# Optimization experiments

Hardware: AMD Instinct MI355X
Metric: run time of the kernel (lower is better)

The kernel has to match this reference:

```python
import jax, jax.numpy as jnp
import numpy as np
from jax import lax

NSTEPS = 7
BN_EPS = 1e-5


def setup_inputs() -> dict:
    key = jax.random.key(0)
    ks = jax.random.split(key, 7)
    bs, in_ch, h, w, k = 8, 16, 256, 256, 3
    f = jax.random.normal(ks[0], (bs, in_ch, h, w), dtype=jnp.float32)
    vec_w = jax.random.normal(ks[1], (2 * in_ch, in_ch, k, k), dtype=jnp.float32) * 0.1
    vec_b = jax.random.normal(ks[2], (2 * in_ch,), dtype=jnp.float32) * 0.1
    bn_gamma = jnp.ones((2 * in_ch,), dtype=jnp.float32)
    bn_beta = jnp.zeros((2 * in_ch,), dtype=jnp.float32)
    fuse_w = jax.random.normal(ks[3], (in_ch, in_ch, NSTEPS, 1, 1), dtype=jnp.float32) * 0.1
    fuse_b = jax.random.normal(ks[4], (in_ch,), dtype=jnp.float32) * 0.1
    return {"f": f, "vec_w": vec_w, "vec_b": vec_b, "bn_gamma": bn_gamma,
            "bn_beta": bn_beta, "fuse_w": fuse_w, "fuse_b": fuse_b}


def _bilinear_sample(src, py, px):
    """Bilinear sample with zero padding (torch grid_sample align_corners=True).
    src: [N,C,H,W]; py,px: [N,H,W] pixel coordinates (row, col)."""
    N, C, H, W = src.shape
    y0 = jnp.floor(py); x0 = jnp.floor(px)
    wy1 = py - y0; wy0 = 1.0 - wy1
    wx1 = px - x0; wx0 = 1.0 - wx1
    src_flat = src.reshape(N, C, H * W)

    def gather(yi, xi):
        valid = (yi >= 0) & (yi <= H - 1) & (xi >= 0) & (xi <= W - 1)
        yc = jnp.clip(yi, 0, H - 1).astype(jnp.int32)
        xc = jnp.clip(xi, 0, W - 1).astype(jnp.int32)
        idx = (yc * W + xc).reshape(N, 1, H * W)
        vals = jnp.take_along_axis(src_flat, idx, axis=2).reshape(N, C, H, W)
        return vals * valid.astype(src.dtype)[:, None, :, :]

    out = (wy0 * wx0)[:, None] * gather(y0, x0) \
        + (wy0 * wx1)[:, None] * gather(y0, x0 + 1) \
        + (wy1 * wx0)[:, None] * gather(y0 + 1, x0) \
        + (wy1 * wx1)[:, None] * gather(y0 + 1, x0 + 1)
    return out


def _warp(src, flow, grid_y, grid_x):
    # grid + flow in pixel space; original normalizes to [-1,1] then grid_sample
    # un-normalizes with align_corners=True, which is exactly pixel coords grid+flow.
    py = grid_y[None] + flow[:, 0]
    px = grid_x[None] + flow[:, 1]
    return _bilinear_sample(src, py, px)


def reference(f, vec_w, vec_b, bn_gamma, bn_beta, fuse_w, fuse_b):
    bs, in_ch, h, w = f.shape
    # vec_conv + BatchNorm2d (training-mode batch stats, biased variance)
    vec = lax.conv_general_dilated(f, vec_w, (1, 1), [(1, 1), (1, 1)],
                                   dimension_numbers=("NCHW", "OIHW", "NCHW"))
    vec = vec + vec_b[None, :, None, None]
    mean = vec.mean(axis=(0, 2, 3))
    var = vec.var(axis=(0, 2, 3))
    vec = bn_gamma[None, :, None, None] * (vec - mean[None, :, None, None]) \
        * lax.rsqrt(var + BN_EPS)[None, :, None, None] + bn_beta[None, :, None, None]

    c = vec.shape[1]  # = 2*in_ch
    vec = vec.reshape(bs * c // 2, 2, h, w)  # per-channel 2D flow fields

    grid_y, grid_x = jnp.meshgrid(jnp.arange(h, dtype=f.dtype),
                                  jnp.arange(w, dtype=f.dtype), indexing="ij")

    # VecInt: scaling and squaring, keeping every intermediate deformation
    vec = vec * (1.0 / 2 ** NSTEPS)
    deforms = []
    for _ in range(NSTEPS):
        vec = vec + _warp(vec, vec, grid_y, grid_x)
        deforms.append(vec)

    fsrc = f.reshape(bs * in_ch, 1, h, w)
    maps = [_warp(fsrc, d, grid_y, grid_x).reshape(bs, in_ch, h, w) for d in deforms]
    stacked = jnp.stack(maps, axis=2)  # [bs, in_ch, nsteps, h, w]

    # Conv3d with kernel (nsteps,1,1) then squeeze -> per-pixel channel/step mix
    out = jnp.einsum("ocs,bcshw->bohw", fuse_w[:, :, :, 0, 0], stacked)
    out = out + fuse_b[None, :, None, None]
    return out
```

## Files before the change

kernel.cpp:

```cpp
#include <hip/hip_runtime.h>
#include <hip/hip_fp16.h>

#define H 256
#define W 256
#define BS 8
#define IC 16
#define OCH 32
#define NSTEPS 7
#define PLANE (H*W)
#define NFIELDS (BS*IC)
#define BN_N (BS*PLANE)
#define BN_EPS 1e-5f
#define PW 260
#define PSZ (260 * 260)

__global__ void transpose_w_kernel(const float* __restrict__ w,
                                   __half2* __restrict__ wTh) {
    for (int idx = threadIdx.x; idx < IC * 9 * 16; idx += blockDim.x) {
        int rc = idx >> 4;
        int p  = idx & 15;
        float lo = w[(2 * p) * (IC * 9) + rc];
        float hi = w[(2 * p + 1) * (IC * 9) + rc];
        wTh[idx] = __floats2half2_rn(lo, hi);
    }
}

__global__ void guard_zero_kernel(unsigned* __restrict__ bufA,
                                  unsigned* __restrict__ bufB,
                                  unsigned short* __restrict__ f16p) {
    int p = blockIdx.x;
    size_t pb = (size_t)p * PSZ;
    for (int i = threadIdx.x; i < 2064; i += blockDim.x) {
        int row, col;
        if (i < 1040) {
            int r = i / 260;
            row = (r == 0) ? 0 : 256 + r;
            col = i - r * 260;
        } else {
            int j = i - 1040;
            int c = j / 256;
            col = (c == 0) ? 0 : 256 + c;
            row = 1 + (j - c * 256);
        }
        size_t off = pb + (size_t)row * PW + col;
        bufA[off] = 0u;
        bufB[off] = 0u;
        f16p[off] = 0;
    }
}

__global__ __launch_bounds__(256) void dup_kernel(const float* __restrict__ f,
                                                  __half* __restrict__ f16p) {
    int blk = blockIdx.x;
    int p  = blk >> 3;
    int r0 = (blk & 7) * 32;
    const float* fp = f + (size_t)p * PLANE;
    __half* dp = f16p + (size_t)p * PSZ;
    int tx = threadIdx.x;
#pragma unroll 4
    for (int ry = 0; ry < 32; ++ry) {
        int y = r0 + ry;
        dp[(size_t)(y + 1) * PW + tx + 1] = __float2half(fp[(size_t)y * W + tx]);
    }
}

__global__ __launch_bounds__(256, 8) void conv_kernel(
    const float* __restrict__ f, const __half2* __restrict__ wTh,
    const float* __restrict__ vec_b, __half2* __restrict__ vec_out) {
    __shared__ __align__(16) __half sf[16][10][40];

    int blk = blockIdx.x;
    int xcd = blk & 7;
    int i   = blk >> 3;
    int b   = i >> 5;
    int j   = i & 31;
    int ty0 = ((xcd << 2) | (j >> 3)) * 8;
    int tx0 = (j & 7) * 32;
    int tid = threadIdx.x;

    {
        int sic = tid >> 4;
        int st  = tid & 15;
        if (st < 10) {
            int gx0 = tx0 - 4 + 4 * st;
            const float* fpl = f + (size_t)(b * IC + sic) * PLANE;
            bool full = (gx0 >= 0) && (gx0 + 3 < W);
#pragma unroll
            for (int r = 0; r < 10; ++r) {
                int gy = ty0 - 1 + r;
                float4 v = make_float4(0.f, 0.f, 0.f, 0.f);
                if ((unsigned)gy < (unsigned)H) {
                    if (full) {
                        v = *(const float4*)(fpl + (size_t)gy * W + gx0);
                    } else {
                        if ((unsigned)(gx0 + 0) < (unsigned)W) v.x = fpl[(size_t)gy * W + gx0 + 0];
                        if ((unsigned)(gx0 + 1) < (unsigned)W) v.y = fpl[(size_t)gy * W + gx0 + 1];
                        if ((unsigned)(gx0 + 2) < (unsigned)W) v.z = fpl[(size_t)gy * W + gx0 + 2];
                        if ((unsigned)(gx0 + 3) < (unsigned)W) v.w = fpl[(size_t)gy * W + gx0 + 3];
                    }
                }
                union { __half2 h[2]; float2 f2; } u;
                u.h[0] = __floats2half2_rn(v.x, v.y);
                u.h[1] = __floats2half2_rn(v.z, v.w);
                *(float2*)&sf[sic][r][4 * st] = u.f2;
            }
        }
    }

    __half2 acc[16];
#pragma unroll
    for (int p = 0; p < 16; ++p)
        acc[p] = __floats2half2_rn(vec_b[2 * p], vec_b[2 * p + 1]);

    __syncthreads();

    int tyl = tid >> 5, txl = tid & 31;
#pragma unroll 2
    for (int ic = 0; ic < 16; ++ic) {
#pragma unroll
        for (int k = 0; k < 9; ++k) {
            int ky = k / 3, kx = k - ky * 3;
            __half2 fv = __half2half2(sf[ic][tyl + ky][txl + kx + 3]);
            const __half2* wrow = wTh + (ic * 9 + k) * 16;
#pragma unroll
            for (int p = 0; p < 16; ++p)
                acc[p] = __hfma2(fv, wrow[p], acc[p]);
        }
    }

    int y = ty0 + tyl, x = tx0 + txl;
#pragma unroll
    for (int c = 0; c < IC; ++c)
        vec_out[(size_t)(b * IC + c) * PLANE + (size_t)y * W + x] = acc[c];
}

__global__ __launch_bounds__(256) void stats_kernel(
    const __half2* __restrict__ vec, float* __restrict__ stats) {
    int blk   = blockIdx.x;
    int n     = blk >> 4;
    int chunk = blk & 15;
    const float4* p4 = (const float4*)(vec + (size_t)n * PLANE + chunk * 4096);
    int tid = threadIdx.x;

    float s0 = 0.f, s1 = 0.f, q0 = 0.f, q1 = 0.f;
#pragma unroll 2
    for (int i = tid; i < 1024; i += 256) {
        float4 w = p4[i];
        const __half2* hh = (const __half2*)&w;
#pragma unroll
        for (int q = 0; q < 4; ++q) {
            float2 v = __half22float2(hh[q]);
            s0 += v.x; s1 += v.y;
            q0 = fmaf(v.x, v.x, q0);
            q1 = fmaf(v.y, v.y, q1);
        }
    }
#pragma unroll
    for (int off = 32; off > 0; off >>= 1) {
        s0 += __shfl_down(s0, off, 64);
        s1 += __shfl_down(s1, off, 64);
        q0 += __shfl_down(q0, off, 64);
        q1 += __shfl_down(q1, off, 64);
    }
    __shared__ float red[4][4];
    int wave = tid >> 6, lane = tid & 63;
    if (lane == 0) {
        red[wave][0] = s0; red[wave][1] = s1;
        red[wave][2] = q0; red[wave][3] = q1;
    }
    __syncthreads();
    if (tid == 0) {
        float t0 = 0.f, t1 = 0.f, t2 = 0.f, t3 = 0.f;
#pragma unroll
        for (int wv = 0; wv < 4; ++wv) {
            t0 += red[wv][0]; t1 += red[wv][1];
            t2 += red[wv][2]; t3 += red[wv][3];
        }
        int ch0 = 2 * (n & 15);
        atomicAdd(stats + ch0,          t0);
        atomicAdd(stats + ch0 + 1,      t1);
        atomicAdd(stats + 32 + ch0,     t2);
        atomicAdd(stats + 32 + ch0 + 1, t3);
    }
}

__global__ void finalize_kernel(const float* __restrict__ stats,
                                const float* __restrict__ gamma,
                                const float* __restrict__ beta,
                                float* __restrict__ AB) {
    int ch = threadIdx.x;
    if (ch < 2 * IC) {
        const float invN = 1.f / (float)BN_N;
        float mean = stats[ch] * invN;
        float var  = stats[32 + ch] * invN - mean * mean;
        float rs   = rsqrtf(var + BN_EPS);
        float a    = gamma[ch] * rs;
        AB[ch]      = a * (1.f / 128.f);
        AB[32 + ch] = (beta[ch] - a * mean) * (1.f / 128.f);
    }
}

__device__ __forceinline__ void tap_setup(float py, float px,
                                          int* o, float* wt) {
    float ffy = floorf(py), ffx = floorf(px);
    int y0 = (int)ffy, x0 = (int)ffx;
    float wy1 = py - ffy, wy0 = 1.f - wy1;
    float wx1 = px - ffx, wx0 = 1.f - wx1;
    bool vy0 = (unsigned)y0 < (unsigned)H, vy1 = (unsigned)(y0 + 1) < (unsigned)H;
    bool vx0 = (unsigned)x0 < (unsigned)W, vx1 = (unsigned)(x0 + 1) < (unsigned)W;
    int yc0 = min(max(y0, 0), H - 1), yc1 = min(max(y0 + 1, 0), H - 1);
    int xc0 = min(max(x0, 0), W - 1), xc1 = min(max(x0 + 1, 0), W - 1);
    o[0] = yc0 * W + xc0; o[1] = yc0 * W + xc1;
    o[2] = yc1 * W + xc0; o[3] = yc1 * W + xc1;
    wt[0] = (vy0 && vx0) ? wy0 * wx0 : 0.f;
    wt[1] = (vy0 && vx1) ? wy0 * wx1 : 0.f;
    wt[2] = (vy1 && vx0) ? wy1 * wx0 : 0.f;
    wt[3] = (vy1 && vx1) ? wy1 * wx1 : 0.f;
}

__device__ __forceinline__ void tap_fast(float py, float px,
                                         int& o, float* wt) {
    float pyc = fminf(fmaxf(py, -1.f), 256.f);
    float pxc = fminf(fmaxf(px, -1.f), 256.f);
    float fy = floorf(pyc), fx = floorf(pxc);
    int y0 = (int)fy, x0 = (int)fx;
    float wy1 = pyc - fy, wy0 = 1.f - wy1;
    float wx1 = pxc - fx, wx0 = 1.f - wx1;
    o = (y0 + 1) * PW + (x0 + 1);
    wt[0] = wy0 * wx0; wt[1] = wy0 * wx1;
    wt[2] = wy1 * wx0; wt[3] = wy1 * wx1;
}

template <bool FIRST, bool LAST>
__global__ __launch_bounds__(256) void step_kernel(
    const __half2* __restrict__ vinRaw, const __half2* __restrict__ vinPad,
    __half2* __restrict__ voutPad, const __half* __restrict__ f16p,
    const float* __restrict__ AB, const float* __restrict__ fw,
    const float* __restrict__ fb, __half* __restrict__ accp,
    float* __restrict__ out, int step) {
    int blk = blockIdx.x;
    int xcd = blk & 7;
    int i   = blk >> 3;
    int b   = i >> 5;
    int h   = (xcd << 5) | (i & 31);
    int tx  = threadIdx.x;
    int idx_raw = h * W + tx;
    int idx_pad = (h + 1) * PW + tx + 1;
    const size_t baseR = (size_t)b * IC * PLANE;
    const size_t baseP = (size_t)b * IC * PSZ;

    float mv[IC];

#pragma unroll 2
    for (int g = 0; g < 4; ++g) {
        float a0j[4], b0j[4], a1j[4], b1j[4];
        float fy[4], fx[4];
        float wt[4][4];
        int   ob[4];
        int   om[4][4];
        const __half2* pl[4];
        float2 vc[4];

#pragma unroll
        for (int j = 0; j < 4; ++j) {
            int c = 4 * g + j;
            if (FIRST) {
                pl[j] = vinRaw + baseR + (size_t)c * PLANE;
                vc[j] = __half22float2(pl[j][idx_raw]);
            } else {
                pl[j] = vinPad + baseP + (size_t)c * PSZ;
                vc[j] = __half22float2(pl[j][idx_pad]);
            }
        }

#pragma unroll
        for (int j = 0; j < 4; ++j) {
            int c = 4 * g + j;
            if (FIRST) {
                a0j[j] = AB[2 * c];     b0j[j] = AB[32 + 2 * c];
                a1j[j] = AB[2 * c + 1]; b1j[j] = AB[32 + 2 * c + 1];
                fy[j] = fmaf(a0j[j], vc[j].x, b0j[j]);
                fx[j] = fmaf(a1j[j], vc[j].y, b1j[j]);
                tap_setup((float)h + fy[j], (float)tx + fx[j], om[j], wt[j]);
            } else {
                fy[j] = vc[j].x;
                fx[j] = vc[j].y;
                tap_fast((float)h + fy[j], (float)tx + fx[j], ob[j], wt[j]);
            }
        }

        float2 t[4][4];
#pragma unroll
        for (int j = 0; j < 4; ++j) {
            if (FIRST) {
#pragma unroll
                for (int k = 0; k < 4; ++k)
                    t[j][k] = __half22float2(pl[j][om[j][k]]);
            } else {
                union { float2 f2; __half2 hh[2]; } top, bot;
                top.f2 = *reinterpret_cast<const float2*>(pl[j] + ob[j]);
                bot.f2 = *reinterpret_cast<const float2*>(pl[j] + ob[j] + PW);
                t[j][0] = __half22float2(top.hh[0]);
                t[j][1] = __half22float2(top.hh[1]);
                t[j][2] = __half22float2(bot.hh[0]);
                t[j][3] = __half22float2(bot.hh[1]);
            }
        }

        float ny[4], nx[4];
        int   pb_[4];
        float pw_[4][4];
#pragma unroll
        for (int j = 0; j < 4; ++j) {
            int c = 4 * g + j;
            float Sy = wt[j][0] * t[j][0].x + wt[j][1] * t[j][1].x
                     + wt[j][2] * t[j][2].x + wt[j][3] * t[j][3].x;
            float Sx = wt[j][0] * t[j][0].y + wt[j][1] * t[j][1].y
                     + wt[j][2] * t[j][2].y + wt[j][3] * t[j][3].y;
            if (FIRST) {
                float Ws = wt[j][0] + wt[j][1] + wt[j][2] + wt[j][3];
                ny[j] = fy[j] + fmaf(a0j[j], Sy, b0j[j] * Ws);
                nx[j] = fx[j] + fmaf(a1j[j], Sx, b1j[j] * Ws);
            } else {
                ny[j] = fy[j] + Sy;
                nx[j] = fx[j] + Sx;
            }
            if (!LAST)
                voutPad[baseP + (size_t)c * PSZ + idx_pad] =
                    __float22half2_rn(make_float2(ny[j], nx[j]));
            tap_fast((float)h + ny[j], (float)tx + nx[j], pb_[j], pw_[j]);
        }

#pragma unroll
        for (int j = 0; j < 4; ++j) {
            int c = 4 * g + j;
            const __half* fp = f16p + baseP + (size_t)c * PSZ;
            union { float f; __half2 h; } r0, r1;
            r0.f = *reinterpret_cast<const float*>(fp + pb_[j]);
            r1.f = *reinterpret_cast<const float*>(fp + pb_[j] + PW);
            float2 g0 = __half22float2(r0.h);
            float2 g1 = __half22float2(r1.h);
            mv[c] = pw_[j][0] * g0.x + pw_[j][1] * g0.y
                  + pw_[j][2] * g1.x + pw_[j][3] * g1.y;
        }
    }

    __half* ap = accp + ((size_t)b * PLANE + idx_raw) * IC;
    float prev[IC];
    if (!FIRST) {
        float4 p0 = ((const float4*)ap)[0];
        float4 p1 = ((const float4*)ap)[1];
        const __half2* ph = (const __half2*)&p0;
#pragma unroll
        for (int k = 0; k < 4; ++k) {
            float2 v = __half22float2(ph[k]);
            prev[2 * k] = v.x; prev[2 * k + 1] = v.y;
        }
        const __half2* qh = (const __half2*)&p1;
#pragma unroll
        for (int k = 0; k < 4; ++k) {
            float2 v = __half22float2(qh[k]);
            prev[8 + 2 * k] = v.x; prev[8 + 2 * k + 1] = v.y;
        }
    }

    float a[IC];
#pragma unroll
    for (int o2 = 0; o2 < IC; ++o2) {
        a[o2] = FIRST ? fb[o2] : prev[o2];
#pragma unroll
        for (int c = 0; c < IC; ++c)
            a[o2] = fmaf(fw[(o2 * IC + c) * NSTEPS + step], mv[c], a[o2]);
    }

    if (LAST) {
#pragma unroll
        for (int o2 = 0; o2 < IC; ++o2)
            out[baseR + (size_t)o2 * PLANE + idx_raw] = a[o2];
    } else {
        float4 s0, s1;
        __half2* sh = (__half2*)&s0;
#pragma unroll
        for (int k = 0; k < 4; ++k)
            sh[k] = __float22half2_rn(make_float2(a[2 * k], a[2 * k + 1]));
        __half2* th = (__half2*)&s1;
#pragma unroll
        for (int k = 0; k < 4; ++k)
            th[k] = __float22half2_rn(make_float2(a[8 + 2 * k], a[9 + 2 * k]));
        ((float4*)ap)[0] = s0;
        ((float4*)ap)[1] = s1;
    }
}

extern "C" void kernel_launch(void* const* d_in, const int* in_sizes, int n_in,
                              void* d_out, int out_size, void* d_ws,
                              size_t ws_size, hipStream_t stream) {
    const float* f      = (const float*)d_in[0];
    const float* vec_w  = (const float*)d_in[1];
    const float* vec_b  = (const float*)d_in[2];
    const float* gamma  = (const float*)d_in[3];
    const float* beta   = (const float*)d_in[4];
    const float* fuse_w = (const float*)d_in[5];
    const float* fuse_b = (const float*)d_in[6];
    float* out = (float*)d_out;

    char* ws = (char*)d_ws;
    const size_t rawB  = (size_t)NFIELDS * PLANE * sizeof(__half2);
    const size_t padB2 = (size_t)NFIELDS * PSZ * sizeof(__half2);
    const size_t padB1 = (size_t)NFIELDS * PSZ * sizeof(__half);
    const size_t accB  = (size_t)NFIELDS * PLANE * sizeof(__half);
    __half2* bufRaw = (__half2*)ws;
    __half2* bufA   = (__half2*)(ws + rawB);
    __half2* bufB   = (__half2*)(ws + rawB + padB2);
    __half*  f16p   = (__half*)(ws + rawB + 2 * padB2);
    __half*  accp   = (__half*)(ws + rawB + 2 * padB2 + padB1);
    __half2* wTh    = (__half2*)(ws + rawB + 2 * padB2 + padB1 + accB);
    float*   stats  = (float*)(wTh + IC * 9 * 16);
    float*   AB     = stats + 64;

    hipMemsetAsync(stats, 0, 64 * sizeof(float), stream);
    transpose_w_kernel<<<1, 512, 0, stream>>>(vec_w, wTh);
    guard_zero_kernel<<<NFIELDS, 256, 0, stream>>>(
        (unsigned*)bufA, (unsigned*)bufB, (unsigned short*)f16p);
    dup_kernel<<<NFIELDS * 8, 256, 0, stream>>>(f, f16p);
    conv_kernel<<<2048, 256, 0, stream>>>(f, wTh, vec_b, bufRaw);
    stats_kernel<<<NFIELDS * 16, 256, 0, stream>>>(bufRaw, stats);
    finalize_kernel<<<1, 64, 0, stream>>>(stats, gamma, beta, AB);

    for (int s = 0; s < NSTEPS; ++s) {
        const __half2* vinPad = (s & 1) ? bufA : bufB;
        __half2*       voutP  = (s & 1) ? bufB : bufA;
        if (s == 0)
            step_kernel<true, false><<<2048, 256, 0, stream>>>(
                bufRaw, (const __half2*)nullptr, bufA, f16p, AB,
                fuse_w, fuse_b, accp, out, s);
        else if (s < NSTEPS - 1)
            step_kernel<false, false><<<2048, 256, 0, stream>>>(
                (const __half2*)nullptr, vinPad, voutP, f16p, AB,
                fuse_w, fuse_b, accp, out, s);
        else
            step_kernel<false, true><<<2048, 256, 0, stream>>>(
                (const __half2*)nullptr, vinPad, (__half2*)nullptr, f16p, AB,
                fuse_w, fuse_b, accp, out, s);
    }
}
```

Before: 502.4 us.

## Split warp steps from channel mix, storing per-step warped maps for a final mix kernel

```diff
diff --git a/kernel.cpp b/kernel.cpp
--- a/kernel.cpp
+++ b/kernel.cpp
@@ -232,6 +232,111 @@
 }
 
 template <bool FIRST, bool LAST>
+__global__ __launch_bounds__(256, 4) void warp_step(
+    const __half2* __restrict__ vinRaw, const __half2* __restrict__ vinPad,
+    __half2* __restrict__ voutPad, const __half* __restrict__ f16p,
+    const float* __restrict__ AB, __half* __restrict__ mvOut) {
+    int blk  = blockIdx.x;
+    int fld  = blk & 127;
+    int band = blk >> 7;
+    int c    = fld & 15;
+    int tx   = threadIdx.x;
+    const __half2* vinR = FIRST ? vinRaw + (size_t)fld * PLANE : nullptr;
+    const __half2* vinP = FIRST ? nullptr : vinPad + (size_t)fld * PSZ;
+    __half2* voutP = LAST ? nullptr : voutPad + (size_t)fld * PSZ;
+    const __half* fp = f16p + (size_t)fld * PSZ;
+    __half* mv = mvOut + (size_t)fld * PLANE;
+
+    float a0 = 0.f, b0 = 0.f, a1 = 0.f, b1 = 0.f;
+    if (FIRST) {
+        a0 = AB[2 * c];     b0 = AB[32 + 2 * c];
+        a1 = AB[2 * c + 1]; b1 = AB[32 + 2 * c + 1];
+    }
+
+#pragma unroll 4
+    for (int r = 0; r < 8; ++r) {
+        int h = band * 8 + r;
+        int idx_raw = h * W + tx;
+        int idx_pad = (h + 1) * PW + tx + 1;
+        float ny, nx;
+        if (FIRST) {
+            float2 vc = __half22float2(vinR[idx_raw]);
+            float fy = fmaf(a0, vc.x, b0);
+            float fx = fmaf(a1, vc.y, b1);
+            int om[4]; float wt[4];
+            tap_setup((float)h + fy, (float)tx + fx, om, wt);
+            float2 t0 = __half22float2(vinR[om[0]]);
+            float2 t1 = __half22float2(vinR[om[1]]);
+            float2 t2 = __half22float2(vinR[om[2]]);
+            float2 t3 = __half22float2(vinR[om[3]]);
+            float Sy = wt[0] * t0.x + wt[1] * t1.x + wt[2] * t2.x + wt[3] * t3.x;
+            float Sx = wt[0] * t0.y + wt[1] * t1.y + wt[2] * t2.y + wt[3] * t3.y;
+            float Ws = wt[0] + wt[1] + wt[2] + wt[3];
+            ny = fy + fmaf(a0, Sy, b0 * Ws);
+            nx = fx + fmaf(a1, Sx, b1 * Ws);
+        } else {
+            float2 vc = __half22float2(vinP[idx_pad]);
+            float fy = vc.x, fx = vc.y;
+            int ob; float wt[4];
+            tap_fast((float)h + fy, (float)tx + fx, ob, wt);
+            union { float2 f2; __half2 hh[2]; } top, bot;
+            top.f2 = *reinterpret_cast<const float2*>(vinP + ob);
+            bot.f2 = *reinterpret_cast<const float2*>(vinP + ob + PW);
+            float2 t0 = __half22float2(top.hh[0]);
+            float2 t1 = __half22float2(top.hh[1]);
+            float2 t2 = __half22float2(bot.hh[0]);
+            float2 t3 = __half22float2(bot.hh[1]);
+            ny = fy + wt[0] * t0.x + wt[1] * t1.x + wt[2] * t2.x + wt[3] * t3.x;
+            nx = fx + wt[0] * t0.y + wt[1] * t1.y + wt[2] * t2.y + wt[3] * t3.y;
+        }
+        if (!LAST)
+            voutP[idx_pad] = __float22half2_rn(make_float2(ny, nx));
+        int pb; float pw[4];
+        tap_fast((float)h + ny, (float)tx + nx, pb, pw);
+        union { float f; __half2 h2; } r0u, r1u;
+        r0u.f = *reinterpret_cast<const float*>(fp + pb);
+        r1u.f = *reinterpret_cast<const float*>(fp + pb + PW);
+        float2 g0 = __half22float2(r0u.h2);
+        float2 g1 = __half22float2(r1u.h2);
+        float m = pw[0] * g0.x + pw[1] * g0.y + pw[2] * g1.x + pw[3] * g1.y;
+        mv[idx_raw] = __float2half(m);
+    }
+}
+
+__global__ __launch_bounds__(256) void mix_kernel(
+    const __half* __restrict__ mvs,
+    const __half* __restrict__ mv6,
+    const float* __restrict__ fw, const float* __restrict__ fb,
+    float* __restrict__ out) {
+    int blk = blockIdx.x;
+    int b   = blk >> 8;
+    int h   = blk & 255;
+    int tx  = threadIdx.x;
+    int idx = h * W + tx;
+
+    float acc[IC];
+#pragma unroll
+    for (int o = 0; o < IC; ++o) acc[o] = fb[o];
+
+#pragma unroll
+    for (int s = 0; s < NSTEPS; ++s) {
+        const __half* base = (s < NSTEPS - 1)
+            ? mvs + (size_t)s * NFIELDS * PLANE : mv6;
+#pragma unroll
+        for (int c = 0; c < IC; ++c) {
+            float m = __half2float(base[(size_t)(b * IC + c) * PLANE + idx]);
+#pragma unroll
+            for (int o = 0; o < IC; ++o)
+                acc[o] = fmaf(fw[(o * IC + c) * NSTEPS + s], m, acc[o]);
+        }
+    }
+
+#pragma unroll
+    for (int o = 0; o < IC; ++o)
+        out[(size_t)(b * IC + o) * PLANE + idx] = acc[o];
+}
+
+template <bool FIRST, bool LAST>
 __global__ __launch_bounds__(256) void step_kernel(
     const __half2* __restrict__ vinRaw, const __half2* __restrict__ vinPad,
     __half2* __restrict__ voutPad, const __half* __restrict__ f16p,
@@ -405,18 +510,26 @@
     float* out = (float*)d_out;
 
     char* ws = (char*)d_ws;
-    const size_t rawB  = (size_t)NFIELDS * PLANE * sizeof(__half2);
-    const size_t padB2 = (size_t)NFIELDS * PSZ * sizeof(__half2);
-    const size_t padB1 = (size_t)NFIELDS * PSZ * sizeof(__half);
-    const size_t accB  = (size_t)NFIELDS * PLANE * sizeof(__half);
+    const size_t rawB   = (size_t)NFIELDS * PLANE * sizeof(__half2);
+    const size_t padB2  = (size_t)NFIELDS * PSZ * sizeof(__half2);
+    const size_t padB1  = (size_t)NFIELDS * PSZ * sizeof(__half);
+    const size_t planeH = (size_t)NFIELDS * PLANE * sizeof(__half);
+    const size_t smallB = 16384;
     __half2* bufRaw = (__half2*)ws;
     __half2* bufA   = (__half2*)(ws + rawB);
     __half2* bufB   = (__half2*)(ws + rawB + padB2);
     __half*  f16p   = (__half*)(ws + rawB + 2 * padB2);
-    __half*  accp   = (__half*)(ws + rawB + 2 * padB2 + padB1);
-    __half2* wTh    = (__half2*)(ws + rawB + 2 * padB2 + padB1 + accB);
-    float*   stats  = (float*)(wTh + IC * 9 * 16);
-    float*   AB     = stats + 64;
+    char*    smallp = ws + rawB + 2 * padB2 + padB1;
+    __half2* wTh    = (__half2*)smallp;
+    float*   stats  = (float*)(smallp + 10240);
+    float*   AB     = (float*)(smallp + 10240 + 256);
+    char*    regionX = smallp + smallB;
+    __half*  mvs    = (__half*)regionX;
+    __half*  accp   = (__half*)regionX;
+
+    const size_t need_new = rawB + 2 * padB2 + padB1 + smallB
+                          + (size_t)(NSTEPS - 1) * planeH;
+    const bool use_new = (ws_size >= need_new);
 
     hipMemsetAsync(stats, 0, 64 * sizeof(float), stream);
     transpose_w_kernel<<<1, 512, 0, stream>>>(vec_w, wTh);
@@ -427,20 +540,41 @@
     stats_kernel<<<NFIELDS * 16, 256, 0, stream>>>(bufRaw, stats);
     finalize_kernel<<<1, 64, 0, stream>>>(stats, gamma, beta, AB);
 
-    for (int s = 0; s < NSTEPS; ++s) {
-        const __half2* vinPad = (s & 1) ? bufA : bufB;
-        __half2*       voutP  = (s & 1) ? bufB : bufA;
-        if (s == 0)
-            step_kernel<true, false><<<2048, 256, 0, stream>>>(
-                bufRaw, (const __half2*)nullptr, bufA, f16p, AB,
-                fuse_w, fuse_b, accp, out, s);
-        else if (s < NSTEPS - 1)
-            step_kernel<false, false><<<2048, 256, 0, stream>>>(
-                (const __half2*)nullptr, vinPad, voutP, f16p, AB,
-                fuse_w, fuse_b, accp, out, s);
-        else
-            step_kernel<false, true><<<2048, 256, 0, stream>>>(
-                (const __half2*)nullptr, vinPad, (__half2*)nullptr, f16p, AB,
-                fuse_w, fuse_b, accp, out, s);
-    }
-}
+    if (use_new) {
+        for (int s = 0; s < NSTEPS; ++s) {
+            const __half2* vinPad = (s & 1) ? bufA : bufB;
+            __half2*       voutP  = (s & 1) ? bufB : bufA;
+            __half* mvP = (s < NSTEPS - 1) ? mvs + (size_t)s * NFIELDS * PLANE
+                                           : (__half*)bufRaw;
+            if (s == 0)
+                warp_step<true, false><<<4096, 256, 0, stream>>>(
+                    bufRaw, (const __half2*)nullptr, bufA, f16p, AB, mvP);
+            else if (s < NSTEPS - 1)
+                warp_step<false, false><<<4096, 256, 0, stream>>>(
+                    (const __half2*)nullptr, vinPad, voutP, f16p, AB, mvP);
+            else
+                warp_step<false, true><<<4096, 256, 0, stream>>>(
+                    (const __half2*)nullptr, vinPad, (__half2*)nullptr, f16p,
+                    AB, mvP);
+        }
+        mix_kernel<<<2048, 256, 0, stream>>>(
+            mvs, (const __half*)bufRaw, fuse_w, fuse_b, out);
+    } else {
+        for (int s = 0; s < NSTEPS; ++s) {
+            const __half2* vinPad = (s & 1) ? bufA : bufB;
+            __half2*       voutP  = (s & 1) ? bufB : bufA;
+            if (s == 0)
+                step_kernel<true, false><<<2048, 256, 0, stream>>>(
+                    bufRaw, (const __half2*)nullptr, bufA, f16p, AB,
+                    fuse_w, fuse_b, accp, out, s);
+            else if (s < NSTEPS - 1)
+                step_kernel<false, false><<<2048, 256, 0, stream>>>(
+                    (const __half2*)nullptr, vinPad, voutP, f16p, AB,
+                    fuse_w, fuse_b, accp, out, s);
+            else
+                step_kernel<false, true><<<2048, 256, 0, stream>>>(
+                    (const __half2*)nullptr, vinPad, (__half2*)nullptr, f16p,
+                    AB, fuse_w, fuse_b, accp, out, s);
+        }
+    }
+}
```

Measured after the change: 580.5 us. 15.5% more time.
